# Optimization experiments

Hardware: AMD Instinct MI355X
Metric: run time of the kernel (lower is better)

## Reference

```python
import jax, jax.numpy as jnp
import numpy as np

L = 28; D = 1024; HQ = 16; HKV = 8; HD = 128; G = HQ // HKV
FF = 3072; VOCAB = 151936; THETA = 1000000.0; EPS = 1e-6
B = 2; PAST = 1024
SCALE = HD ** -0.5


def _rmsnorm(x, w):
    v = jnp.mean(jnp.square(x), axis=-1, keepdims=True)
    return x * jax.lax.rsqrt(v + EPS) * w


def _rotate_half(x):
    x1, x2 = jnp.split(x, 2, axis=-1)
    return jnp.concatenate([-x2, x1], axis=-1)


def setup_inputs() -> dict:
    key = jax.random.key(0)
    ks = jax.random.split(key, 12)
    s = 0.02
    return {
        "input_embeds": jax.random.normal(ks[0], (B, 1, D), jnp.float32),
        "position_ids": jax.random.randint(ks[1], (B, 1), 0, PAST).astype(jnp.int32),
        "past_keys": jax.random.normal(ks[2], (L, B, HKV, PAST, HD), jnp.float32),
        "past_values": jax.random.normal(ks[3], (L, B, HKV, PAST, HD), jnp.float32),
        "Wq": s * jax.random.normal(ks[4], (L, D, HQ * HD), jnp.float32),
        "Wk": s * jax.random.normal(ks[5], (L, D, HKV * HD), jnp.float32),
        "Wv": s * jax.random.normal(ks[6], (L, D, HKV * HD), jnp.float32),
        "Wo": s * jax.random.normal(ks[7], (L, HQ * HD, D), jnp.float32),
        "Wg": s * jax.random.normal(ks[8], (L, D, FF), jnp.float32),
        "Wu": s * jax.random.normal(ks[9], (L, D, FF), jnp.float32),
        "Wd": s * jax.random.normal(ks[10], (L, FF, D), jnp.float32),
        "ln1_w": jnp.ones((L, D), jnp.float32),
        "ln2_w": jnp.ones((L, D), jnp.float32),
        "qn_w": jnp.ones((L, HD), jnp.float32),
        "kn_w": jnp.ones((L, HD), jnp.float32),
        "final_norm_w": jnp.ones((D,), jnp.float32),
        "lm_head_w": s * jax.random.normal(ks[11], (D, VOCAB), jnp.float32),
    }


def reference(input_embeds, position_ids, past_keys, past_values,
              Wq, Wk, Wv, Wo, Wg, Wu, Wd,
              ln1_w, ln2_w, qn_w, kn_w, final_norm_w, lm_head_w):
    # Rotary embeddings for the single new position.
    pos = position_ids.astype(jnp.float32)                      # [B,1]
    inv_freq = 1.0 / (THETA ** (jnp.arange(0, HD, 2, dtype=jnp.float32) / HD))
    freqs = pos[..., None] * inv_freq                           # [B,1,HD/2]
    emb = jnp.concatenate([freqs, freqs], axis=-1)              # [B,1,HD]
    cos = jnp.cos(emb)[:, None, :, :]                           # [B,1,1,HD] (head bcast)
    sin = jnp.sin(emb)[:, None, :, :]

    def layer(h, xs):
        wq, wk, wv, wo, wg, wu, wd, l1, l2, qw, kw, pk, pv = xs
        n = _rmsnorm(h, l1)                                     # [B,1,D]
        q = _rmsnorm((n @ wq).reshape(B, 1, HQ, HD), qw).transpose(0, 2, 1, 3)   # [B,HQ,1,HD]
        k = _rmsnorm((n @ wk).reshape(B, 1, HKV, HD), kw).transpose(0, 2, 1, 3)  # [B,HKV,1,HD]
        v = (n @ wv).reshape(B, 1, HKV, HD).transpose(0, 2, 1, 3)
        q = q * cos + _rotate_half(q) * sin
        k = k * cos + _rotate_half(k) * sin
        K = jnp.concatenate([pk, k], axis=2)                    # [B,HKV,PAST+1,HD]
        V = jnp.concatenate([pv, v], axis=2)
        # GQA without materializing repeated KV: q heads grouped kv-major,
        # matching torch _repeat_kv head ordering (head = kv*G + g).
        qg = q[:, :, 0, :].reshape(B, HKV, G, HD)
        scores = jnp.einsum('bkgd,bksd->bkgs', qg, K) * SCALE
        w = jax.nn.softmax(scores.astype(jnp.float32), axis=-1).astype(q.dtype)
        o = jnp.einsum('bkgs,bksd->bkgd', w, V).reshape(B, 1, HQ * HD)
        h = h + o @ wo
        m = _rmsnorm(h, l2)
        h = h + (jax.nn.silu(m @ wg) * (m @ wu)) @ wd           # SwiGLU MLP
        return h, (K, V)

    xs = (Wq, Wk, Wv, Wo, Wg, Wu, Wd, ln1_w, ln2_w, qn_w, kn_w, past_keys, past_values)
    h, (present_keys, present_values) = jax.lax.scan(layer, input_embeds, xs)
    logits = _rmsnorm(h, final_norm_w) @ lm_head_w              # [B,1,VOCAB]
    return logits, present_keys, present_values
```

## Files before the change

kernel.cpp:

```cpp
#include <hip/hip_runtime.h>
#include <math.h>

#define NL 28
#define DIM 1024
#define NHQ 16
#define NHKV 8
#define HDIM 128
#define NG 2
#define NFF 3072
#define NVOCAB 151936
#define NB 2
#define NPAST 1024
#define NPTOT 1025
#define EPSF 1e-6f
#define QKSCALE 0.08838834764831845f
#define LOGTHETA 13.815510557964274f

#define SQKV 8
#define SCH 32

#define OFF_N1   0
#define OFF_H    2048
#define OFF_H1   4096
#define OFF_QKV  8192
#define OFF_AM   73728
#define OFF_AL   74752
#define OFF_AO   75776
#define OFF_WO   206848
#define OFF_G    223232
#define OFF_U    272384
#define OFF_WD   321536

#define PK_OFF ((size_t)NB*NVOCAB)
#define PV_OFF (PK_OFF + (size_t)NL*NB*NHKV*NPTOT*HDIM)

__device__ __forceinline__ float wave_red_sum(float v) {
  #pragma unroll
  for (int off = 32; off > 0; off >>= 1) v += __shfl_xor(v, off);
  return v;
}

__global__ __launch_bounds__(256) void k0_init(const float* __restrict__ embeds,
    const float* __restrict__ ln1, float* __restrict__ ws)
{
  int tid = threadIdx.x;
  int lane = tid & 63, w = tid >> 6;
  __shared__ float wr[8];
  int d = tid*4;
  float4 v0 = *(const float4*)(embeds + d);
  float4 v1 = *(const float4*)(embeds + DIM + d);
  float4 lw = *(const float4*)(ln1 + d);
  *(float4*)(ws + OFF_H + d) = v0;
  *(float4*)(ws + OFF_H + DIM + d) = v1;
  float s0 = wave_red_sum(v0.x*v0.x + v0.y*v0.y + v0.z*v0.z + v0.w*v0.w);
  float s1 = wave_red_sum(v1.x*v1.x + v1.y*v1.y + v1.z*v1.z + v1.w*v1.w);
  if (lane == 0) { wr[w] = s0; wr[4+w] = s1; }
  __syncthreads();
  float r0 = rsqrtf((wr[0]+wr[1]+wr[2]+wr[3])/DIM + EPSF);
  float r1 = rsqrtf((wr[4]+wr[5]+wr[6]+wr[7])/DIM + EPSF);
  float4 n0 = make_float4(v0.x*r0*lw.x, v0.y*r0*lw.y, v0.z*r0*lw.z, v0.w*r0*lw.w);
  float4 n1 = make_float4(v1.x*r1*lw.x, v1.y*r1*lw.y, v1.z*r1*lw.z, v1.w*r1*lw.w);
  *(float4*)(ws + OFF_N1 + d) = n0;
  *(float4*)(ws + OFF_N1 + DIM + d) = n1;
}

__global__ __launch_bounds__(256) void k1_qkv(
    const float* __restrict__ Wq_, const float* __restrict__ Wk_,
    const float* __restrict__ Wv_, const float* __restrict__ ln1,
    float* __restrict__ ws, int l)
{
  int bx = blockIdx.x, by = blockIdx.y;
  int tid = threadIdx.x;
  int lane = tid & 63, w = tid >> 6;
  __shared__ __align__(16) float sh[NB][128];
  __shared__ __align__(16) float red[256*9];
  __shared__ float wr[8];

  int ct = tid & 15, rs = tid >> 4;
  int colg = bx*64 + ct*4;
  const float* W; int O; int wcol;
  if (bx < 32)      { W = Wq_; O = 2048; wcol = colg; }
  else if (bx < 48) { W = Wk_; O = 1024; wcol = colg - 2048; }
  else              { W = Wv_; O = 1024; wcol = colg - 3072; }
  int r0 = rs*8;
  const float* Wp = W + (size_t)l*DIM*O + (size_t)(by*128 + r0)*O + wcol;
  float4 wb[8];

  if (l == 0) {
    int b = tid >> 7, r = tid & 127;
    float nv = ws[OFF_N1 + b*DIM + by*128 + r];
    __builtin_amdgcn_sched_barrier(0);
    #pragma unroll
    for (int i = 0; i < 8; i++) wb[i] = *(const float4*)(Wp + (size_t)i*O);
    sh[b][r] = nv;
    __syncthreads();
  } else {
    int d = tid*4;
    float4 a0 = *(const float4*)(ws + OFF_H1 + d);
    float4 a1 = *(const float4*)(ws + OFF_H1 + DIM + d);
    #pragma unroll
    for (int s = 0; s < 8; s++) {
      float4 p0 = *(const float4*)(ws + OFF_WD + (s*NB + 0)*DIM + d);
      float4 p1 = *(const float4*)(ws + OFF_WD + (s*NB + 1)*DIM + d);
      a0.x += p0.x; a0.y += p0.y; a0.z += p0.z; a0.w += p0.w;
      a1.x += p1.x; a1.y += p1.y; a1.z += p1.z; a1.w += p1.w;
    }
    float4 lw = *(const float4*)(ln1 + (size_t)l*DIM + d);
    __builtin_amdgcn_sched_barrier(0);
    #pragma unroll
    for (int i = 0; i < 8; i++) wb[i] = *(const float4*)(Wp + (size_t)i*O);
    if (bx == 0 && by == 0) {
      *(float4*)(ws + OFF_H + d) = a0;
      *(float4*)(ws + OFF_H + DIM + d) = a1;
    }
    float s0 = wave_red_sum(a0.x*a0.x + a0.y*a0.y + a0.z*a0.z + a0.w*a0.w);
    float s1 = wave_red_sum(a1.x*a1.x + a1.y*a1.y + a1.z*a1.z + a1.w*a1.w);
    if (lane == 0) { wr[w] = s0; wr[4+w] = s1; }
    __syncthreads();
    float rq0 = rsqrtf((wr[0]+wr[1]+wr[2]+wr[3])/DIM + EPSF);
    float rq1 = rsqrtf((wr[4]+wr[5]+wr[6]+wr[7])/DIM + EPSF);
    int r = d - by*128;
    if (r >= 0 && r < 128) {
      sh[0][r] = a0.x*rq0*lw.x; sh[0][r+1] = a0.y*rq0*lw.y;
      sh[0][r+2] = a0.z*rq0*lw.z; sh[0][r+3] = a0.w*rq0*lw.w;
      sh[1][r] = a1.x*rq1*lw.x; sh[1][r+1] = a1.y*rq1*lw.y;
      sh[1][r+2] = a1.z*rq1*lw.z; sh[1][r+3] = a1.w*rq1*lw.w;
    }
    __syncthreads();
  }

  float a[2][4] = {};
  #pragma unroll
  for (int i = 0; i < 8; i++) {
    float x0 = sh[0][r0+i], x1 = sh[1][r0+i];
    a[0][0] += x0*wb[i].x; a[0][1] += x0*wb[i].y; a[0][2] += x0*wb[i].z; a[0][3] += x0*wb[i].w;
    a[1][0] += x1*wb[i].x; a[1][1] += x1*wb[i].y; a[1][2] += x1*wb[i].z; a[1][3] += x1*wb[i].w;
  }
  float* rp = red + tid*9;
  #pragma unroll
  for (int e = 0; e < 4; e++) { rp[e] = a[0][e]; rp[4+e] = a[1][e]; }
  __syncthreads();
  if (tid < 16) {
    float o[8] = {};
    #pragma unroll
    for (int j = 0; j < 16; j++) {
      const float* q = red + (size_t)(j*16 + tid)*9;
      #pragma unroll
      for (int e = 0; e < 8; e++) o[e] += q[e];
    }
    int cg = bx*64 + tid*4;
    #pragma unroll
    for (int e = 0; e < 4; e++) {
      ws[OFF_QKV + (by*NB + 0)*4096 + cg + e] = o[e];
      ws[OFF_QKV + (by*NB + 1)*4096 + cg + e] = o[4+e];
    }
  }
}

__global__ __launch_bounds__(256) void k2_attn(
    const float* __restrict__ pastK, const float* __restrict__ pastV,
    const int* __restrict__ posids, const float* __restrict__ qnw,
    const float* __restrict__ knw, float* __restrict__ out,
    float* __restrict__ ws, int l)
{
  int c = blockIdx.x, kv = blockIdx.y, b = blockIdx.z;
  int tid = threadIdx.x;
  int lane = tid & 63, w = tid >> 6;
  int g = tid >> 7, o = tid & 127;
  __shared__ __align__(16) float qf[NG][HDIM];
  __shared__ __align__(16) float kf[HDIM];
  __shared__ __align__(16) float vf[HDIM];
  __shared__ __align__(16) float pre[NG][HDIM];
  __shared__ __align__(16) float kpre[HDIM];
  __shared__ __align__(16) float po[8][NG][HDIM];
  __shared__ float wr[8];
  __shared__ float pm[8][NG], pl[8][NG];

  int hq = kv*NG + g;
  float qp = 0.f, kp = 0.f;
  #pragma unroll
  for (int s = 0; s < SQKV; s++) qp += ws[OFF_QKV + (s*NB + b)*4096 + hq*HDIM + o];
  int kvslot = g ? 3072 : 2048;
  #pragma unroll
  for (int s = 0; s < SQKV; s++) kp += ws[OFF_QKV + (s*NB + b)*4096 + kvslot + kv*HDIM + o];
  float qw_ = qnw[l*HDIM + o];
  float kw_ = knw[l*HDIM + o];
  float pos = (float)posids[b];
  __builtin_amdgcn_sched_barrier(0);

  int grp = tid >> 5, q = tid & 31;
  int p0 = c*32;
  int p1 = (c == SCH-1) ? NPTOT : p0 + 32;
  size_t pastbase = ((((size_t)l*NB + b)*NHKV + kv)*NPAST)*HDIM;
  size_t presbase = ((((size_t)l*NB + b)*NHKV + kv)*NPTOT)*HDIM;
  float4 kk[5], vv[5];
  int ns = 0;
  for (int p = p0 + grp; p < p1; p += 8) {
    if (p < NPAST) {
      kk[ns] = *(const float4*)(pastK + pastbase + (size_t)p*HDIM + q*4);
      vv[ns] = *(const float4*)(pastV + pastbase + (size_t)p*HDIM + q*4);
    }
    ns++;
  }
  __builtin_amdgcn_sched_barrier(0);

  float sq = wave_red_sum(qp*qp);
  float sk = wave_red_sum(kp*kp);
  if (lane == 0) { wr[w] = sq; wr[4+w] = sk; }
  __syncthreads();
  float qss = wr[g<<1] + wr[(g<<1)+1];
  float qr = rsqrtf(qss/HDIM + EPSF);
  float kss = wr[4] + wr[5];
  float kr = rsqrtf(kss/HDIM + EPSF);
  float qn = qp*qr*qw_;
  pre[g][o] = qn;
  if (g == 0) kpre[o] = kp*kr*kw_;
  else vf[o] = kp;
  __syncthreads();
  float ang = pos * expf(-(2.0f*(float)(o & 63)/(float)HDIM)*LOGTHETA);
  float sn, cs;
  sincosf(ang, &sn, &cs);
  {
    float rotq = (o < 64) ? -pre[g][o+64] : pre[g][o-64];
    qf[g][o] = qn*cs + rotq*sn;
    if (g == 0) {
      float kx = kpre[o];
      float rotk = (o < 64) ? -kpre[o+64] : kpre[o-64];
      kf[o] = kx*cs + rotk*sn;
    }
  }
  __syncthreads();

  float4 q0 = *(const float4*)&qf[0][q*4];
  float4 q1 = *(const float4*)&qf[1][q*4];
  float sc0[5], sc1[5];
  int i = 0;
  for (int p = p0 + grp; p < p1; p += 8, i++) {
    float4 k4, v4;
    if (p < NPAST) { k4 = kk[i]; v4 = vv[i]; }
    else { k4 = *(const float4*)&kf[q*4]; v4 = *(const float4*)&vf[q*4]; vv[i] = v4; }
    *(float4*)(out + PK_OFF + presbase + (size_t)p*HDIM + q*4) = k4;
    *(float4*)(out + PV_OFF + presbase + (size_t)p*HDIM + q*4) = v4;
    float d0 = q0.x*k4.x + q0.y*k4.y + q0.z*k4.z + q0.w*k4.w;
    float d1 = q1.x*k4.x + q1.y*k4.y + q1.z*k4.z + q1.w*k4.w;
    #pragma unroll
    for (int off = 16; off > 0; off >>= 1) {
      d0 += __shfl_xor(d0, off);
      d1 += __shfl_xor(d1, off);
    }
    sc0[i] = d0*QKSCALE; sc1[i] = d1*QKSCALE;
  }
  float m0 = -1e30f, m1 = -1e30f;
  for (int j = 0; j < i; j++) { m0 = fmaxf(m0, sc0[j]); m1 = fmaxf(m1, sc1[j]); }
  if (q == 0) { pm[grp][0] = m0; pm[grp][1] = m1; }
  __syncthreads();
  float M0 = -1e30f, M1 = -1e30f;
  #pragma unroll
  for (int j = 0; j < 8; j++) { M0 = fmaxf(M0, pm[j][0]); M1 = fmaxf(M1, pm[j][1]); }
  float l0 = 0.f, l1 = 0.f;
  float4 o0 = {0,0,0,0}, o1 = {0,0,0,0};
  for (int j = 0; j < i; j++) {
    float w0 = __expf(sc0[j] - M0), w1 = __expf(sc1[j] - M1);
    l0 += w0; l1 += w1;
    o0.x += w0*vv[j].x; o0.y += w0*vv[j].y; o0.z += w0*vv[j].z; o0.w += w0*vv[j].w;
    o1.x += w1*vv[j].x; o1.y += w1*vv[j].y; o1.z += w1*vv[j].z; o1.w += w1*vv[j].w;
  }
  if (q == 0) { pl[grp][0] = l0; pl[grp][1] = l1; }
  *(float4*)&po[grp][0][q*4] = o0;
  *(float4*)&po[grp][1][q*4] = o1;
  __syncthreads();
  {
    int head = tid >> 7, dd = tid & 127;
    float acc = 0.f;
    #pragma unroll
    for (int j = 0; j < 8; j++) acc += po[j][head][dd];
    int base = ((b*NHKV + kv)*NG + head)*SCH + c;
    ws[OFF_AO + (size_t)base*HDIM + dd] = acc;
    if (dd == 0) {
      float ll = 0.f;
      #pragma unroll
      for (int j = 0; j < 8; j++) ll += pl[j][head];
      ws[OFF_AM + base] = (head ? M1 : M0);
      ws[OFF_AL + base] = ll;
    }
  }
}

__global__ __launch_bounds__(256) void k3_wo(const float* __restrict__ Wo_,
    float* __restrict__ ws, int l)
{
  int bx = blockIdx.x, by = blockIdx.y;
  int tid = threadIdx.x;
  __shared__ __align__(16) float x[NB][256];
  __shared__ float wf[NB][2][SCH];
  __shared__ float invL[NB][2];
  __shared__ __align__(16) float red[256*9];

  if (tid < 128) {
    int b = tid >> 6, hh = (tid >> 5) & 1, cc = tid & 31;
    int hb = b*16 + by*2 + hh;
    float m  = ws[OFF_AM + hb*SCH + cc];
    float ll = ws[OFF_AL + hb*SCH + cc];
    float M = m;
    #pragma unroll
    for (int off = 16; off > 0; off >>= 1) M = fmaxf(M, __shfl_xor(M, off));
    float f = __expf(m - M);
    float Ls = ll*f;
    #pragma unroll
    for (int off = 16; off > 0; off >>= 1) Ls += __shfl_xor(Ls, off);
    wf[b][hh][cc] = f;
    if (cc == 0) invL[b][hh] = 1.0f/Ls;
  }
  __builtin_amdgcn_sched_barrier(0);

  int ct = tid & 7, rs = tid >> 3;
  int col = bx*32 + ct*4;
  int r0 = rs*8;
  const float* Wp = Wo_ + (size_t)l*(NHQ*HDIM)*DIM + (size_t)(by*256 + r0)*DIM + col;
  float4 wb[8];
  #pragma unroll
  for (int i = 0; i < 8; i++) wb[i] = *(const float4*)(Wp + (size_t)i*DIM);
  __syncthreads();

  for (int e = tid; e < 512; e += 256) {
    int b = e >> 8, rr = e & 255, hh = rr >> 7, dd = rr & 127;
    int hb = b*16 + by*2 + hh;
    const float* op = ws + OFF_AO + (size_t)(hb*SCH)*HDIM + dd;
    float acc = 0.f;
    #pragma unroll
    for (int cc = 0; cc < SCH; cc++) acc += op[(size_t)cc*HDIM]*wf[b][hh][cc];
    x[b][rr] = acc*invL[b][hh];
  }
  __syncthreads();
  float a[2][4] = {};
  #pragma unroll
  for (int i = 0; i < 8; i++) {
    float x0 = x[0][r0+i], x1 = x[1][r0+i];
    a[0][0] += x0*wb[i].x; a[0][1] += x0*wb[i].y; a[0][2] += x0*wb[i].z; a[0][3] += x0*wb[i].w;
    a[1][0] += x1*wb[i].x; a[1][1] += x1*wb[i].y; a[1][2] += x1*wb[i].z; a[1][3] += x1*wb[i].w;
  }
  float* rp = red + tid*9;
  #pragma unroll
  for (int e = 0; e < 4; e++) { rp[e] = a[0][e]; rp[4+e] = a[1][e]; }
  __syncthreads();
  if (tid < 8) {
    float o[8] = {};
    #pragma unroll
    for (int j = 0; j < 32; j++) {
      const float* qq = red + (size_t)(j*8 + tid)*9;
      #pragma unroll
      for (int e = 0; e < 8; e++) o[e] += qq[e];
    }
    int cg = bx*32 + tid*4;
    #pragma unroll
    for (int e = 0; e < 4; e++) {
      ws[OFF_WO + (by*NB + 0)*DIM + cg + e] = o[e];
      ws[OFF_WO + (by*NB + 1)*DIM + cg + e] = o[4+e];
    }
  }
}

__global__ __launch_bounds__(256) void k4_mlp1(const float* __restrict__ Wg_,
    const float* __restrict__ Wu_, const float* __restrict__ ln2,
    float* __restrict__ ws, int l)
{
  int bx = blockIdx.x, by = blockIdx.y;
  int tid = threadIdx.x;
  int lane = tid & 63, w = tid >> 6;
  __shared__ __align__(16) float sh[NB][128];
  __shared__ __align__(16) float red[256*9];
  __shared__ float wr[8];

  int d = tid*4;
  float4 a0 = *(const float4*)(ws + OFF_H + d);
  float4 a1 = *(const float4*)(ws + OFF_H + DIM + d);
  #pragma unroll
  for (int s = 0; s < 8; s++) {
    float4 p0 = *(const float4*)(ws + OFF_WO + (s*NB + 0)*DIM + d);
    float4 p1 = *(const float4*)(ws + OFF_WO + (s*NB + 1)*DIM + d);
    a0.x += p0.x; a0.y += p0.y; a0.z += p0.z; a0.w += p0.w;
    a1.x += p1.x; a1.y += p1.y; a1.z += p1.z; a1.w += p1.w;
  }
  float4 lw = *(const float4*)(ln2 + (size_t)l*DIM + d);
  __builtin_amdgcn_sched_barrier(0);

  int ct = tid & 15, rs = tid >> 4;
  int col = bx*64 + ct*4;
  int r0 = rs*8;
  const float* Wgp = Wg_ + (size_t)l*DIM*NFF + (size_t)(by*128 + r0)*NFF + col;
  const float* Wup = Wu_ + (size_t)l*DIM*NFF + (size_t)(by*128 + r0)*NFF + col;
  float4 wg[8], wu[8];
  #pragma unroll
  for (int i = 0; i < 8; i++) {
    wg[i] = *(const float4*)(Wgp + (size_t)i*NFF);
    wu[i] = *(const float4*)(Wup + (size_t)i*NFF);
  }

  if (bx == 0 && by == 0) {
    *(float4*)(ws + OFF_H1 + d) = a0;
    *(float4*)(ws + OFF_H1 + DIM + d) = a1;
  }
  float s0 = wave_red_sum(a0.x*a0.x + a0.y*a0.y + a0.z*a0.z + a0.w*a0.w);
  float s1 = wave_red_sum(a1.x*a1.x + a1.y*a1.y + a1.z*a1.z + a1.w*a1.w);
  if (lane == 0) { wr[w] = s0; wr[4+w] = s1; }
  __syncthreads();
  float rq0 = rsqrtf((wr[0]+wr[1]+wr[2]+wr[3])/DIM + EPSF);
  float rq1 = rsqrtf((wr[4]+wr[5]+wr[6]+wr[7])/DIM + EPSF);
  int r = d - by*128;
  if (r >= 0 && r < 128) {
    sh[0][r] = a0.x*rq0*lw.x; sh[0][r+1] = a0.y*rq0*lw.y;
    sh[0][r+2] = a0.z*rq0*lw.z; sh[0][r+3] = a0.w*rq0*lw.w;
    sh[1][r] = a1.x*rq1*lw.x; sh[1][r+1] = a1.y*rq1*lw.y;
    sh[1][r+2] = a1.z*rq1*lw.z; sh[1][r+3] = a1.w*rq1*lw.w;
  }
  __syncthreads();

  float ag[2][4] = {}, au[2][4] = {};
  #pragma unroll
  for (int i = 0; i < 8; i++) {
    float x0 = sh[0][r0+i], x1 = sh[1][r0+i];
    ag[0][0] += x0*wg[i].x; ag[0][1] += x0*wg[i].y; ag[0][2] += x0*wg[i].z; ag[0][3] += x0*wg[i].w;
    ag[1][0] += x1*wg[i].x; ag[1][1] += x1*wg[i].y; ag[1][2] += x1*wg[i].z; ag[1][3] += x1*wg[i].w;
    au[0][0] += x0*wu[i].x; au[0][1] += x0*wu[i].y; au[0][2] += x0*wu[i].z; au[0][3] += x0*wu[i].w;
    au[1][0] += x1*wu[i].x; au[1][1] += x1*wu[i].y; au[1][2] += x1*wu[i].z; au[1][3] += x1*wu[i].w;
  }
  float* rp = red + tid*9;
  #pragma unroll
  for (int e = 0; e < 4; e++) { rp[e] = ag[0][e]; rp[4+e] = ag[1][e]; }
  __syncthreads();
  if (tid < 16) {
    float o[8] = {};
    #pragma unroll
    for (int j = 0; j < 16; j++) {
      const float* qq = red + (size_t)(j*16 + tid)*9;
      #pragma unroll
      for (int e = 0; e < 8; e++) o[e] += qq[e];
    }
    int cg = bx*64 + tid*4;
    #pragma unroll
    for (int e = 0; e < 4; e++) {
      ws[OFF_G + (by*NB + 0)*NFF + cg + e] = o[e];
      ws[OFF_G + (by*NB + 1)*NFF + cg + e] = o[4+e];
    }
  }
  __syncthreads();
  #pragma unroll
  for (int e = 0; e < 4; e++) { rp[e] = au[0][e]; rp[4+e] = au[1][e]; }
  __syncthreads();
  if (tid < 16) {
    float o[8] = {};
    #pragma unroll
    for (int j = 0; j < 16; j++) {
      const float* qq = red + (size_t)(j*16 + tid)*9;
      #pragma unroll
      for (int e = 0; e < 8; e++) o[e] += qq[e];
    }
    int cg = bx*64 + tid*4;
    #pragma unroll
    for (int e = 0; e < 4; e++) {
      ws[OFF_U + (by*NB + 0)*NFF + cg + e] = o[e];
      ws[OFF_U + (by*NB + 1)*NFF + cg + e] = o[4+e];
    }
  }
}

__global__ __launch_bounds__(256) void k5_mlp2(const float* __restrict__ Wd_,
    float* __restrict__ ws, int l)
{
  int bx = blockIdx.x, by = blockIdx.y;
  int tid = threadIdx.x;
  __shared__ __align__(16) float act[NB][384];
  __shared__ __align__(16) float red[256*9];

  float4 gacc = {0,0,0,0}, uacc = {0,0,0,0};
  int pb = 0, pf4 = 0;
  if (tid < 192) {
    pb = tid / 96; pf4 = tid % 96;
    int f4 = (by*384)/4 + pf4;
    const float4* Gp = (const float4*)(ws + OFF_G);
    const float4* Up = (const float4*)(ws + OFF_U);
    #pragma unroll
    for (int s = 0; s < 8; s++) {
      float4 g4 = Gp[(size_t)(s*NB + pb)*(NFF/4) + f4];
      float4 u4 = Up[(size_t)(s*NB + pb)*(NFF/4) + f4];
      gacc.x += g4.x; gacc.y += g4.y; gacc.z += g4.z; gacc.w += g4.w;
      uacc.x += u4.x; uacc.y += u4.y; uacc.z += u4.z; uacc.w += u4.w;
    }
  }
  __builtin_amdgcn_sched_barrier(0);

  int ct = tid & 7, rs = tid >> 3;
  int col = bx*32 + ct*4;
  int r0 = rs*12;
  const float* Wp = Wd_ + (size_t)l*NFF*DIM + (size_t)(by*384 + r0)*DIM + col;
  float4 wb[12];
  #pragma unroll
  for (int i = 0; i < 12; i++) wb[i] = *(const float4*)(Wp + (size_t)i*DIM);

  if (tid < 192) {
    float4 r;
    r.x = (gacc.x / (1.0f + __expf(-gacc.x)))*uacc.x;
    r.y = (gacc.y / (1.0f + __expf(-gacc.y)))*uacc.y;
    r.z = (gacc.z / (1.0f + __expf(-gacc.z)))*uacc.z;
    r.w = (gacc.w / (1.0f + __expf(-gacc.w)))*uacc.w;
    *(float4*)&act[pb][pf4*4] = r;
  }
  __syncthreads();

  float a[2][4] = {};
  #pragma unroll
  for (int i = 0; i < 12; i++) {
    float x0 = act[0][r0+i], x1 = act[1][r0+i];
    a[0][0] += x0*wb[i].x; a[0][1] += x0*wb[i].y; a[0][2] += x0*wb[i].z; a[0][3] += x0*wb[i].w;
    a[1][0] += x1*wb[i].x; a[1][1] += x1*wb[i].y; a[1][2] += x1*wb[i].z; a[1][3] += x1*wb[i].w;
  }
  float* rp = red + tid*9;
  #pragma unroll
  for (int e = 0; e < 4; e++) { rp[e] = a[0][e]; rp[4+e] = a[1][e]; }
  __syncthreads();
  if (tid < 8) {
    float o[8] = {};
    #pragma unroll
    for (int j = 0; j < 32; j++) {
      const float* qq = red + (size_t)(j*8 + tid)*9;
      #pragma unroll
      for (int e = 0; e < 8; e++) o[e] += qq[e];
    }
    int cg = bx*32 + tid*4;
    #pragma unroll
    for (int e = 0; e < 4; e++) {
      ws[OFF_WD + (by*NB + 0)*DIM + cg + e] = o[e];
      ws[OFF_WD + (by*NB + 1)*DIM + cg + e] = o[4+e];
    }
  }
}

__global__ __launch_bounds__(256) void k6_lmhead(const float* __restrict__ lmw,
    const float* __restrict__ fnw, const float* __restrict__ ws,
    float* __restrict__ out)
{
  __shared__ __align__(16) float nf[NB*DIM];
  __shared__ __align__(16) float red[256*9];
  __shared__ float wr[8];
  int tid = threadIdx.x;
  int lane = tid & 63, w = tid >> 6;

  int d = tid*4;
  float4 a0 = *(const float4*)(ws + OFF_H1 + d);
  float4 a1 = *(const float4*)(ws + OFF_H1 + DIM + d);
  #pragma unroll
  for (int s = 0; s < 8; s++) {
    float4 p0 = *(const float4*)(ws + OFF_WD + (s*NB + 0)*DIM + d);
    float4 p1 = *(const float4*)(ws + OFF_WD + (s*NB + 1)*DIM + d);
    a0.x += p0.x; a0.y += p0.y; a0.z += p0.z; a0.w += p0.w;
    a1.x += p1.x; a1.y += p1.y; a1.z += p1.z; a1.w += p1.w;
  }
  float4 fw = *(const float4*)(fnw + d);
  __builtin_amdgcn_sched_barrier(0);

  float s0 = wave_red_sum(a0.x*a0.x + a0.y*a0.y + a0.z*a0.z + a0.w*a0.w);
  float s1 = wave_red_sum(a1.x*a1.x + a1.y*a1.y + a1.z*a1.z + a1.w*a1.w);
  if (lane == 0) { wr[w] = s0; wr[4+w] = s1; }
  __syncthreads();
  float rq0 = rsqrtf((wr[0]+wr[1]+wr[2]+wr[3])/DIM + EPSF);
  float rq1 = rsqrtf((wr[4]+wr[5]+wr[6]+wr[7])/DIM + EPSF);
  nf[d]   = a0.x*rq0*fw.x; nf[d+1] = a0.y*rq0*fw.y;
  nf[d+2] = a0.z*rq0*fw.z; nf[d+3] = a0.w*rq0*fw.w;
  nf[DIM+d]   = a1.x*rq1*fw.x; nf[DIM+d+1] = a1.y*rq1*fw.y;
  nf[DIM+d+2] = a1.z*rq1*fw.z; nf[DIM+d+3] = a1.w*rq1*fw.w;
  __syncthreads();

  int ct = tid & 15, rs = tid >> 4;
  int col = blockIdx.x*64 + ct*4;
  const float* Wp = lmw + (size_t)(rs*64)*NVOCAB + col;
  float a[2][4] = {};
  for (int t = 0; t < 8; t++) {
    float4 wb[8];
    #pragma unroll
    for (int i = 0; i < 8; i++)
      wb[i] = *(const float4*)(Wp + (size_t)(t*8 + i)*NVOCAB);
    #pragma unroll
    for (int i = 0; i < 8; i++) {
      int rr = rs*64 + t*8 + i;
      float x0 = nf[rr], x1 = nf[DIM+rr];
      a[0][0] += x0*wb[i].x; a[0][1] += x0*wb[i].y; a[0][2] += x0*wb[i].z; a[0][3] += x0*wb[i].w;
      a[1][0] += x1*wb[i].x; a[1][1] += x1*wb[i].y; a[1][2] += x1*wb[i].z; a[1][3] += x1*wb[i].w;
    }
  }
  float* rp = red + tid*9;
  #pragma unroll
  for (int e = 0; e < 4; e++) { rp[e] = a[0][e]; rp[4+e] = a[1][e]; }
  __syncthreads();
  if (tid < 16) {
    float o[8] = {};
    #pragma unroll
    for (int j = 0; j < 16; j++) {
      const float* qq = red + (size_t)(j*16 + tid)*9;
      #pragma unroll
      for (int e = 0; e < 8; e++) o[e] += qq[e];
    }
    int cg = blockIdx.x*64 + tid*4;
    #pragma unroll
    for (int e = 0; e < 4; e++) {
      out[cg + e] = o[e];
      out[NVOCAB + cg + e] = o[4+e];
    }
  }
}

extern "C" void kernel_launch(void* const* d_in, const int* in_sizes, int n_in,
                              void* d_out, int out_size, void* d_ws, size_t ws_size,
                              hipStream_t stream) {
  (void)in_sizes; (void)n_in; (void)out_size; (void)ws_size;
  const float* embeds = (const float*)d_in[0];
  const int*   posids = (const int*)d_in[1];
  const float* pastK  = (const float*)d_in[2];
  const float* pastV  = (const float*)d_in[3];
  const float* Wq     = (const float*)d_in[4];
  const float* Wk     = (const float*)d_in[5];
  const float* Wv     = (const float*)d_in[6];
  const float* Wo     = (const float*)d_in[7];
  const float* Wg     = (const float*)d_in[8];
  const float* Wu     = (const float*)d_in[9];
  const float* Wd     = (const float*)d_in[10];
  const float* ln1    = (const float*)d_in[11];
  const float* ln2    = (const float*)d_in[12];
  const float* qnw    = (const float*)d_in[13];
  const float* knw    = (const float*)d_in[14];
  const float* fnw    = (const float*)d_in[15];
  const float* lmw    = (const float*)d_in[16];
  float* out = (float*)d_out;
  float* ws  = (float*)d_ws;

  k0_init<<<1, 256, 0, stream>>>(embeds, ln1, ws);
  for (int l = 0; l < NL; l++) {
    k1_qkv <<<dim3(64, 8), 256, 0, stream>>>(Wq, Wk, Wv, ln1, ws, l);
    k2_attn<<<dim3(SCH, NHKV, NB), 256, 0, stream>>>(pastK, pastV, posids, qnw, knw, out, ws, l);
    k3_wo  <<<dim3(32, 8), 256, 0, stream>>>(Wo, ws, l);
    k4_mlp1<<<dim3(48, 8), 256, 0, stream>>>(Wg, Wu, ln2, ws, l);
    k5_mlp2<<<dim3(32, 8), 256, 0, stream>>>(Wd, ws, l);
  }
  k6_lmhead<<<NVOCAB/64, 256, 0, stream>>>(lmw, fnw, ws, out);
}
```

Baseline: 1.406 ms.

## Move past KV cache copy into QKV kernel blocks and split final norm

Extra blocks appended to the QKV projection grid copy the past K/V cache into the present outputs. The attention kernel then only reads past K/V and writes just the new token's row, which lets its loop become a fixed, unrolled 4-iteration body plus a separate term for the new token. The final RMSNorm is moved into its own single-block kernel so the many lm_head blocks no longer each recompute it. The aim is to overlap the memory-bound cache copy with the weight-streaming GEMV and to cut redundant work, at the cost of one extra launch and more bandwidth contention inside k1.

```diff
diff --git a/kernel.cpp b/kernel.cpp
--- a/kernel.cpp
+++ b/kernel.cpp
@@ -18,6 +18,7 @@
 
 #define SQKV 8
 #define SCH 32
+#define NCOPY 128
 
 #define OFF_N1   0
 #define OFF_H    2048
@@ -33,6 +34,8 @@
 
 #define PK_OFF ((size_t)NB*NVOCAB)
 #define PV_OFF (PK_OFF + (size_t)NL*NB*NHKV*NPTOT*HDIM)
+#define PK4 (PK_OFF/4)
+#define PV4 (PV_OFF/4)
 
 __device__ __forceinline__ float wave_red_sum(float v) {
   #pragma unroll
@@ -67,10 +70,28 @@
 __global__ __launch_bounds__(256) void k1_qkv(
     const float* __restrict__ Wq_, const float* __restrict__ Wk_,
     const float* __restrict__ Wv_, const float* __restrict__ ln1,
-    float* __restrict__ ws, int l)
-{
-  int bx = blockIdx.x, by = blockIdx.y;
-  int tid = threadIdx.x;
+    const float* __restrict__ pastK, const float* __restrict__ pastV,
+    float* __restrict__ out, float* __restrict__ ws, int l)
+{
+  int bid = blockIdx.x;
+  int tid = threadIdx.x;
+  if (bid >= 512) {
+    int cb = bid - 512;
+    const float4* pk4 = (const float4*)pastK;
+    const float4* pv4 = (const float4*)pastV;
+    float4* o4 = (float4*)out;
+    #pragma unroll
+    for (int t = 0; t < 16; t++) {
+      size_t idx = (size_t)(t*NCOPY + cb)*256 + tid;
+      size_t pair = idx >> 15, j = idx & 32767;
+      size_t sbase = ((size_t)l*16 + pair)*32768 + j;
+      size_t dbase = ((size_t)l*16 + pair)*32800 + j;
+      o4[PK4 + dbase] = pk4[sbase];
+      o4[PV4 + dbase] = pv4[sbase];
+    }
+    return;
+  }
+  int bx = bid & 63, by = bid >> 6;
   int lane = tid & 63, w = tid >> 6;
   __shared__ __align__(16) float sh[NB][128];
   __shared__ __align__(16) float red[256*9];
@@ -190,17 +211,16 @@
 
   int grp = tid >> 5, q = tid & 31;
   int p0 = c*32;
-  int p1 = (c == SCH-1) ? NPTOT : p0 + 32;
-  size_t pastbase = ((((size_t)l*NB + b)*NHKV + kv)*NPAST)*HDIM;
+  size_t pastb4 = ((((size_t)l*NB + b)*NHKV + kv)*NPAST)*(HDIM/4);
   size_t presbase = ((((size_t)l*NB + b)*NHKV + kv)*NPTOT)*HDIM;
-  float4 kk[5], vv[5];
-  int ns = 0;
-  for (int p = p0 + grp; p < p1; p += 8) {
-    if (p < NPAST) {
-      kk[ns] = *(const float4*)(pastK + pastbase + (size_t)p*HDIM + q*4);
-      vv[ns] = *(const float4*)(pastV + pastbase + (size_t)p*HDIM + q*4);
-    }
-    ns++;
+  const float4* pk4 = (const float4*)pastK;
+  const float4* pv4 = (const float4*)pastV;
+  float4 kk[4], vv[4];
+  #pragma unroll
+  for (int i = 0; i < 4; i++) {
+    size_t p = p0 + grp + i*8;
+    kk[i] = pk4[pastb4 + p*(HDIM/4) + q];
+    vv[i] = pv4[pastb4 + p*(HDIM/4) + q];
   }
   __builtin_amdgcn_sched_barrier(0);
 
@@ -208,10 +228,8 @@
   float sk = wave_red_sum(kp*kp);
   if (lane == 0) { wr[w] = sq; wr[4+w] = sk; }
   __syncthreads();
-  float qss = wr[g<<1] + wr[(g<<1)+1];
-  float qr = rsqrtf(qss/HDIM + EPSF);
-  float kss = wr[4] + wr[5];
-  float kr = rsqrtf(kss/HDIM + EPSF);
+  float qr = rsqrtf((wr[g<<1] + wr[(g<<1)+1])/HDIM + EPSF);
+  float kr = rsqrtf((wr[4] + wr[5])/HDIM + EPSF);
   float qn = qp*qr*qw_;
   pre[g][o] = qn;
   if (g == 0) kpre[o] = kp*kr*kw_;
@@ -233,16 +251,11 @@
 
   float4 q0 = *(const float4*)&qf[0][q*4];
   float4 q1 = *(const float4*)&qf[1][q*4];
-  float sc0[5], sc1[5];
-  int i = 0;
-  for (int p = p0 + grp; p < p1; p += 8, i++) {
-    float4 k4, v4;
-    if (p < NPAST) { k4 = kk[i]; v4 = vv[i]; }
-    else { k4 = *(const float4*)&kf[q*4]; v4 = *(const float4*)&vf[q*4]; vv[i] = v4; }
-    *(float4*)(out + PK_OFF + presbase + (size_t)p*HDIM + q*4) = k4;
-    *(float4*)(out + PV_OFF + presbase + (size_t)p*HDIM + q*4) = v4;
-    float d0 = q0.x*k4.x + q0.y*k4.y + q0.z*k4.z + q0.w*k4.w;
-    float d1 = q1.x*k4.x + q1.y*k4.y + q1.z*k4.z + q1.w*k4.w;
+  float sc0[4], sc1[4];
+  #pragma unroll
+  for (int i = 0; i < 4; i++) {
+    float d0 = q0.x*kk[i].x + q0.y*kk[i].y + q0.z*kk[i].z + q0.w*kk[i].w;
+    float d1 = q1.x*kk[i].x + q1.y*kk[i].y + q1.z*kk[i].z + q1.w*kk[i].w;
     #pragma unroll
     for (int off = 16; off > 0; off >>= 1) {
       d0 += __shfl_xor(d0, off);
@@ -250,8 +263,25 @@
     }
     sc0[i] = d0*QKSCALE; sc1[i] = d1*QKSCALE;
   }
-  float m0 = -1e30f, m1 = -1e30f;
-  for (int j = 0; j < i; j++) { m0 = fmaxf(m0, sc0[j]); m1 = fmaxf(m1, sc1[j]); }
+  float xs0 = -1e30f, xs1 = -1e30f;
+  float4 xv = make_float4(0.f, 0.f, 0.f, 0.f);
+  if (c == SCH-1 && grp == 0) {
+    float4 kX = *(const float4*)&kf[q*4];
+    xv = *(const float4*)&vf[q*4];
+    *(float4*)(out + PK_OFF + presbase + (size_t)NPAST*HDIM + q*4) = kX;
+    *(float4*)(out + PV_OFF + presbase + (size_t)NPAST*HDIM + q*4) = xv;
+    float d0 = q0.x*kX.x + q0.y*kX.y + q0.z*kX.z + q0.w*kX.w;
+    float d1 = q1.x*kX.x + q1.y*kX.y + q1.z*kX.z + q1.w*kX.w;
+    #pragma unroll
+    for (int off = 16; off > 0; off >>= 1) {
+      d0 += __shfl_xor(d0, off);
+      d1 += __shfl_xor(d1, off);
+    }
+    xs0 = d0*QKSCALE; xs1 = d1*QKSCALE;
+  }
+  float m0 = fmaxf(fmaxf(sc0[0], sc0[1]), fmaxf(sc0[2], sc0[3]));
+  float m1 = fmaxf(fmaxf(sc1[0], sc1[1]), fmaxf(sc1[2], sc1[3]));
+  m0 = fmaxf(m0, xs0); m1 = fmaxf(m1, xs1);
   if (q == 0) { pm[grp][0] = m0; pm[grp][1] = m1; }
   __syncthreads();
   float M0 = -1e30f, M1 = -1e30f;
@@ -259,11 +289,18 @@
   for (int j = 0; j < 8; j++) { M0 = fmaxf(M0, pm[j][0]); M1 = fmaxf(M1, pm[j][1]); }
   float l0 = 0.f, l1 = 0.f;
   float4 o0 = {0,0,0,0}, o1 = {0,0,0,0};
-  for (int j = 0; j < i; j++) {
+  #pragma unroll
+  for (int j = 0; j < 4; j++) {
     float w0 = __expf(sc0[j] - M0), w1 = __expf(sc1[j] - M1);
     l0 += w0; l1 += w1;
     o0.x += w0*vv[j].x; o0.y += w0*vv[j].y; o0.z += w0*vv[j].z; o0.w += w0*vv[j].w;
     o1.x += w1*vv[j].x; o1.y += w1*vv[j].y; o1.z += w1*vv[j].z; o1.w += w1*vv[j].w;
+  }
+  {
+    float w0 = __expf(xs0 - M0), w1 = __expf(xs1 - M1);
+    l0 += w0; l1 += w1;
+    o0.x += w0*xv.x; o0.y += w0*xv.y; o0.z += w0*xv.z; o0.w += w0*xv.w;
+    o1.x += w1*xv.x; o1.y += w1*xv.y; o1.z += w1*xv.z; o1.w += w1*xv.w;
   }
   if (q == 0) { pl[grp][0] = l0; pl[grp][1] = l1; }
   *(float4*)&po[grp][0][q*4] = o0;
@@ -535,16 +572,12 @@
   }
 }
 
-__global__ __launch_bounds__(256) void k6_lmhead(const float* __restrict__ lmw,
-    const float* __restrict__ fnw, const float* __restrict__ ws,
-    float* __restrict__ out)
-{
-  __shared__ __align__(16) float nf[NB*DIM];
-  __shared__ __align__(16) float red[256*9];
+__global__ __launch_bounds__(256) void kf_final(const float* __restrict__ fnw,
+    float* __restrict__ ws)
+{
+  int tid = threadIdx.x;
+  int lane = tid & 63, w = tid >> 6;
   __shared__ float wr[8];
-  int tid = threadIdx.x;
-  int lane = tid & 63, w = tid >> 6;
-
   int d = tid*4;
   float4 a0 = *(const float4*)(ws + OFF_H1 + d);
   float4 a1 = *(const float4*)(ws + OFF_H1 + DIM + d);
@@ -556,18 +589,26 @@
     a1.x += p1.x; a1.y += p1.y; a1.z += p1.z; a1.w += p1.w;
   }
   float4 fw = *(const float4*)(fnw + d);
-  __builtin_amdgcn_sched_barrier(0);
-
   float s0 = wave_red_sum(a0.x*a0.x + a0.y*a0.y + a0.z*a0.z + a0.w*a0.w);
   float s1 = wave_red_sum(a1.x*a1.x + a1.y*a1.y + a1.z*a1.z + a1.w*a1.w);
   if (lane == 0) { wr[w] = s0; wr[4+w] = s1; }
   __syncthreads();
   float rq0 = rsqrtf((wr[0]+wr[1]+wr[2]+wr[3])/DIM + EPSF);
   float rq1 = rsqrtf((wr[4]+wr[5]+wr[6]+wr[7])/DIM + EPSF);
-  nf[d]   = a0.x*rq0*fw.x; nf[d+1] = a0.y*rq0*fw.y;
-  nf[d+2] = a0.z*rq0*fw.z; nf[d+3] = a0.w*rq0*fw.w;
-  nf[DIM+d]   = a1.x*rq1*fw.x; nf[DIM+d+1] = a1.y*rq1*fw.y;
-  nf[DIM+d+2] = a1.z*rq1*fw.z; nf[DIM+d+3] = a1.w*rq1*fw.w;
+  float4 n0 = make_float4(a0.x*rq0*fw.x, a0.y*rq0*fw.y, a0.z*rq0*fw.z, a0.w*rq0*fw.w);
+  float4 n1 = make_float4(a1.x*rq1*fw.x, a1.y*rq1*fw.y, a1.z*rq1*fw.z, a1.w*rq1*fw.w);
+  *(float4*)(ws + OFF_N1 + d) = n0;
+  *(float4*)(ws + OFF_N1 + DIM + d) = n1;
+}
+
+__global__ __launch_bounds__(256) void k6_lmhead(const float* __restrict__ lmw,
+    const float* __restrict__ ws, float* __restrict__ out)
+{
+  __shared__ __align__(16) float nf[NB*DIM];
+  __shared__ __align__(16) float red[256*9];
+  int tid = threadIdx.x;
+  *(float4*)&nf[tid*4]        = *(const float4*)(ws + OFF_N1 + tid*4);
+  *(float4*)&nf[1024 + tid*4] = *(const float4*)(ws + OFF_N1 + 1024 + tid*4);
   __syncthreads();
 
   int ct = tid & 15, rs = tid >> 4;
@@ -634,11 +675,12 @@
 
   k0_init<<<1, 256, 0, stream>>>(embeds, ln1, ws);
   for (int l = 0; l < NL; l++) {
-    k1_qkv <<<dim3(64, 8), 256, 0, stream>>>(Wq, Wk, Wv, ln1, ws, l);
+    k1_qkv <<<512 + NCOPY, 256, 0, stream>>>(Wq, Wk, Wv, ln1, pastK, pastV, out, ws, l);
     k2_attn<<<dim3(SCH, NHKV, NB), 256, 0, stream>>>(pastK, pastV, posids, qnw, knw, out, ws, l);
     k3_wo  <<<dim3(32, 8), 256, 0, stream>>>(Wo, ws, l);
     k4_mlp1<<<dim3(48, 8), 256, 0, stream>>>(Wg, Wu, ln2, ws, l);
     k5_mlp2<<<dim3(32, 8), 256, 0, stream>>>(Wd, ws, l);
   }
-  k6_lmhead<<<NVOCAB/64, 256, 0, stream>>>(lmw, fnw, ws, out);
-}
+  kf_final<<<1, 256, 0, stream>>>(fnw, ws);
+  k6_lmhead<<<NVOCAB/64, 256, 0, stream>>>(lmw, ws, out);
+}
```

Result: faster. 1.321 ms (-6.0%).
